# Optimization experiments

Hardware: AMD Instinct MI355X
Metric: run time of the kernel (lower is better)

The kernel has to match this reference:

```python
import jax, jax.numpy as jnp
import numpy as np

B, D, STRIDE, OUT = 8192, 1024, 16, 64
L = D // STRIDE


def setup_inputs() -> dict:
    key = jax.random.key(0)
    kx, kw, kb = jax.random.split(key, 3)
    x = jax.random.normal(kx, (B, D), dtype=jnp.float32)
    # Stacked per-layer Dense kernels: layer i only sees features j < i*STRIDE.
    # Glorot-ish scale; masked entries are zeroed in reference() (faithful: they
    # don't exist in the original per-layer kernels).
    W = jax.random.normal(kw, (L, D, OUT), dtype=jnp.float32) * 0.02
    b = jax.random.normal(kb, (L, OUT), dtype=jnp.float32) * 0.02
    return {"x": x, "W": W, "b": b}


def reference(x, W, b):
    # Original: tf.stack([Dense_i(x[..., :i*stride]) for i in range(L)], -2)
    # Equivalent single causal-masked batched matmul.
    Lx, Dx, Ox = W.shape
    stride = Dx // Lx
    # mask[l, d] = 1 if feature d is visible to layer l (d < l*stride)
    mask = (jnp.arange(Dx)[None, :] < (jnp.arange(Lx) * stride)[:, None]).astype(W.dtype)
    Wm = W * mask[:, :, None]                      # [L, D, O]
    out = jnp.einsum("bd,ldo->blo", x, Wm) + b    # [B, L, O]
    return out
```

## Files before the change

### kernel.cpp

```cpp
#include <hip/hip_runtime.h>
#include <hip/hip_bf16.h>
#include <stdint.h>

#define BROWS 8192
#define DDIM  1024
#define LDIM  64
#define ODIM  64
#define NDIM  4096
#define KSTRIDE 16

typedef __attribute__((ext_vector_type(8))) short bf16x8;
typedef __attribute__((ext_vector_type(4))) float f32x4;
typedef __attribute__((ext_vector_type(8))) unsigned short u16x8;

static __device__ __forceinline__ unsigned short f2bf(float f) {
    union { float f; uint32_t u; } v; v.f = f;
    uint32_t r = 0x7FFFu + ((v.u >> 16) & 1u);
    return (unsigned short)((v.u + r) >> 16);
}

static __device__ __forceinline__ void async16(const void* g, void* l) {
    __builtin_amdgcn_global_load_lds(
        (const __attribute__((address_space(1))) void*)g,
        (__attribute__((address_space(3))) void*)l, 16, 0, 0);
}

__global__ __launch_bounds__(256) void prep_kernel(const float* __restrict__ x,
                                                   const float* __restrict__ W,
                                                   unsigned short* __restrict__ xb,
                                                   unsigned short* __restrict__ wbt) {
    const int bid = blockIdx.x;
    if (bid < 1024) {
        __shared__ float tile[64][65];
        const int l  = bid >> 4;
        const int d0 = (bid & 15) << 6;
        const int t  = threadIdx.x;
        {
            const int dd = t >> 2;
            const int o4 = (t & 3) << 4;
            const float* src = W + ((size_t)((l << 10) + d0 + dd) << 6) + o4;
            #pragma unroll
            for (int j = 0; j < 4; ++j) {
                float4 v = reinterpret_cast<const float4*>(src)[j];
                tile[dd][o4 + 4 * j + 0] = v.x;
                tile[dd][o4 + 4 * j + 1] = v.y;
                tile[dd][o4 + 4 * j + 2] = v.z;
                tile[dd][o4 + 4 * j + 3] = v.w;
            }
        }
        __syncthreads();
        {
            const int o    = t >> 2;
            const int dloc = (t & 3) << 4;
            const int kmax = l * KSTRIDE;
            unsigned short* dst = wbt + ((size_t)((l << 6) + o) << 10) + d0 + dloc;
            u16x8 r0, r1;
            #pragma unroll
            for (int j = 0; j < 8; ++j) {
                int da = d0 + dloc + j;
                int db = da + 8;
                r0[j] = (da < kmax) ? f2bf(tile[dloc + j][o])     : (unsigned short)0;
                r1[j] = (db < kmax) ? f2bf(tile[dloc + 8 + j][o]) : (unsigned short)0;
            }
            *reinterpret_cast<u16x8*>(dst)     = r0;
            *reinterpret_cast<u16x8*>(dst + 8) = r1;
        }
    } else {
        int i = (bid - 1024) * 256 + threadIdx.x;
        const float4* xf = reinterpret_cast<const float4*>(x);
        float4 v0 = xf[2 * i];
        float4 v1 = xf[2 * i + 1];
        u16x8 r;
        r[0] = f2bf(v0.x); r[1] = f2bf(v0.y); r[2] = f2bf(v0.z); r[3] = f2bf(v0.w);
        r[4] = f2bf(v1.x); r[5] = f2bf(v1.y); r[6] = f2bf(v1.z); r[7] = f2bf(v1.w);
        reinterpret_cast<u16x8*>(xb)[i] = r;
    }
}

#define MMQ(A, B) \
    _Pragma("unroll") \
    for (int m = 0; m < 4; ++m) \
    _Pragma("unroll") \
    for (int n = 0; n < 4; ++n) \
        acc[m][n] = __builtin_amdgcn_mfma_f32_16x16x32_bf16(A[m], B[n], acc[m][n], 0, 0, 0);

#define READF(T, A, B) do { \
    const char* pb_ = lds + ((T) % 3) * 24576; \
    _Pragma("unroll") \
    for (int m = 0; m < 4; ++m) A[m] = *reinterpret_cast<const bf16x8*>(pb_ + aoff + m * 1024); \
    _Pragma("unroll") \
    for (int n = 0; n < 4; ++n) B[n] = *reinterpret_cast<const bf16x8*>(pb_ + boff + n * 1024); \
} while (0)

#define PHASE(T, Acur, Bcur, Anxt, Bnxt) \
    asm volatile("s_waitcnt vmcnt(3)" ::: "memory");    \
    __builtin_amdgcn_sched_barrier(0); \
    __builtin_amdgcn_s_barrier();                       \
    stage((T) + 3);                                     \
    READF((T) + 1, Anxt, Bnxt);                         \
    __builtin_amdgcn_sched_barrier(0); \
    __builtin_amdgcn_s_setprio(1); \
    MMQ(Acur, Bcur); \
    __builtin_amdgcn_s_setprio(0); \
    asm volatile("s_waitcnt lgkmcnt(0)" ::: "memory");

__global__ __launch_bounds__(512)
__attribute__((amdgpu_waves_per_eu(2)))
void ar_gemm_kernel(const unsigned short* __restrict__ xb,
                    const unsigned short* __restrict__ wbt,
                    const float* __restrict__ bias,
                    float* __restrict__ out) {
    __shared__ char lds[73728];

    const int s  = blockIdx.x >> 8;
    const int i  = blockIdx.x & 255;
    const int bm = ((s & 1) << 4) + (i & 15);
    const int bn = ((s < 2) ? 16 : 0) + 15 - (i >> 4);
    const int tid  = threadIdx.x;
    const int lane = tid & 63;
    const int wid  = tid >> 6;
    const int wm   = wid >> 1;
    const int wn   = wid & 1;

    const int nkt = bn + 1;

    const int cb = (tid & 3) << 4;
    const char* gA = (const char*)xb  + ((size_t)((bm << 8) + (tid >> 2)) << 11) + cb;
    const char* gB = (const char*)wbt + ((size_t)((bn << 7) + (tid >> 2)) << 11) + cb;

    const int aoff = ((wm << 6) + (lane & 15)) * 64 + ((lane >> 4) << 4);
    const int boff = 16384 + ((wn << 6) + (lane & 15)) * 64 + ((lane >> 4) << 4);

    f32x4 acc[4][4];
    #pragma unroll
    for (int m = 0; m < 4; ++m)
        #pragma unroll
        for (int n = 0; n < 4; ++n)
            acc[m][n] = (f32x4)(0.f);

    bf16x8 aA[4], bA[4], aB[4], bB[4];

    auto stage = [&](int t) {
        const int kb = (t < nkt ? t : nkt - 1) << 6;
        char* l = lds + (t % 3) * 24576 + tid * 16;
        async16(gA + kb, l);
        async16(gA + ((size_t)128 << 11) + kb, l + 8192);
        async16(gB + kb, l + 16384);
    };

    stage(0); stage(1); stage(2);
    asm volatile("s_waitcnt vmcnt(6)" ::: "memory");
    __builtin_amdgcn_s_barrier();
    READF(0, aA, bA);
    asm volatile("s_waitcnt lgkmcnt(0)" ::: "memory");

    int t = 0;
    while (true) {
        PHASE(t, aA, bA, aB, bB);
        if (++t >= nkt) break;
        PHASE(t, aB, bB, aA, bA);
        if (++t >= nkt) break;
    }
    asm volatile("s_waitcnt vmcnt(0)" ::: "memory");

    const int crow = (bm << 8) + (wm << 6) + ((lane >> 4) << 2);
    const int ccol = (bn << 7) + (wn << 6) + (lane & 15);
    float bv[4];
    #pragma unroll
    for (int n = 0; n < 4; ++n) bv[n] = bias[ccol + n * 16];
    #pragma unroll
    for (int m = 0; m < 4; ++m)
        #pragma unroll
        for (int n = 0; n < 4; ++n)
            #pragma unroll
            for (int j = 0; j < 4; ++j)
                out[(size_t)(crow + m * 16 + j) * NDIM + ccol + n * 16] = acc[m][n][j] + bv[n];
}

__global__ __launch_bounds__(256) void naive_kernel(const float* __restrict__ x,
                                                    const float* __restrict__ W,
                                                    const float* __restrict__ bias,
                                                    float* __restrict__ out) {
    size_t idx = (size_t)blockIdx.x * 256 + threadIdx.x;
    if (idx >= (size_t)BROWS * NDIM) return;
    int m = (int)(idx >> 12);
    int n = (int)(idx & 4095);
    int l = n >> 6;
    int o = n & 63;
    int kmax = l * KSTRIDE;
    float s = bias[n];
    const float* xr = x + (size_t)m * DDIM;
    const float* wp = W + ((size_t)l << 16) + o;
    for (int d = 0; d < kmax; ++d) s += xr[d] * wp[(size_t)d << 6];
    out[idx] = s;
}

extern "C" void kernel_launch(void* const* d_in, const int* in_sizes, int n_in,
                              void* d_out, int out_size, void* d_ws, size_t ws_size,
                              hipStream_t stream) {
    const float* x = (const float*)d_in[0];
    const float* W = (const float*)d_in[1];
    const float* b = (const float*)d_in[2];
    float* out = (float*)d_out;

    const size_t need = ((size_t)BROWS * DDIM + (size_t)NDIM * DDIM) * sizeof(unsigned short);
    if (ws_size < need) {
        int total = BROWS * NDIM;
        naive_kernel<<<(total + 255) / 256, 256, 0, stream>>>(x, W, b, out);
        return;
    }
    unsigned short* xbuf = (unsigned short*)d_ws;
    unsigned short* wbt  = xbuf + (size_t)BROWS * DDIM;

    prep_kernel<<<5120, 256, 0, stream>>>(x, W, xbuf, wbt);
    ar_gemm_kernel<<<1024, 512, 0, stream>>>(xbuf, wbt, b, out);
}
```

Before: 69.59 us.

## Shrink GEMM tile to 128x128, load B fragments straight from global into registers

The GEMM moves from 256x128 tiles with 512 threads to 128x128 tiles with 256 threads, and the grid doubles to 2048 blocks. Only the A (x) tile is staged through LDS with async loads into a 3-deep buffer. Each wave now reads its B (weight) fragments directly from global memory into double-buffered registers. This cuts LDS use and traffic and should allow more resident blocks per CU. In exchange, the weight tile is no longer shared between waves through LDS, so global loads of W rise, and the smaller tiles lower arithmetic intensity.

```diff
diff --git a/kernel.cpp b/kernel.cpp
--- a/kernel.cpp
+++ b/kernel.cpp
@@ -77,45 +77,38 @@
     }
 }
 
-#define MMQ(A, B) \
+#define ITER(T, BC, BN) do { \
+    stageA((T) + 2);                                    \
+    loadB((T) + 1, BN);                                 \
+    const char* pb_ = lds + ((T) % 3) * 8192; \
+    bf16x8 a[4]; \
+    _Pragma("unroll") \
+    for (int m = 0; m < 4; ++m) a[m] = *reinterpret_cast<const bf16x8*>(pb_ + aoff + m * 1024); \
+    __builtin_amdgcn_s_setprio(1); \
     _Pragma("unroll") \
     for (int m = 0; m < 4; ++m) \
-    _Pragma("unroll") \
-    for (int n = 0; n < 4; ++n) \
-        acc[m][n] = __builtin_amdgcn_mfma_f32_16x16x32_bf16(A[m], B[n], acc[m][n], 0, 0, 0);
-
-#define READF(T, A, B) do { \
-    const char* pb_ = lds + ((T) % 3) * 24576; \
-    _Pragma("unroll") \
-    for (int m = 0; m < 4; ++m) A[m] = *reinterpret_cast<const bf16x8*>(pb_ + aoff + m * 1024); \
-    _Pragma("unroll") \
-    for (int n = 0; n < 4; ++n) B[n] = *reinterpret_cast<const bf16x8*>(pb_ + boff + n * 1024); \
+        _Pragma("unroll") \
+        for (int n = 0; n < 4; ++n) \
+            acc[m][n] = __builtin_amdgcn_mfma_f32_16x16x32_bf16(a[m], BC[n], acc[m][n], 0, 0, 0); \
+    __builtin_amdgcn_s_setprio(0); \
+    asm volatile("s_waitcnt lgkmcnt(0)" ::: "memory");  \
+    asm volatile("s_waitcnt vmcnt(6)" ::: "memory");    \
+    __builtin_amdgcn_sched_barrier(0); \
+    __builtin_amdgcn_s_barrier(); \
+    __builtin_amdgcn_sched_barrier(0); \
 } while (0)
 
-#define PHASE(T, Acur, Bcur, Anxt, Bnxt) \
-    asm volatile("s_waitcnt vmcnt(3)" ::: "memory");    \
-    __builtin_amdgcn_sched_barrier(0); \
-    __builtin_amdgcn_s_barrier();                       \
-    stage((T) + 3);                                     \
-    READF((T) + 1, Anxt, Bnxt);                         \
-    __builtin_amdgcn_sched_barrier(0); \
-    __builtin_amdgcn_s_setprio(1); \
-    MMQ(Acur, Bcur); \
-    __builtin_amdgcn_s_setprio(0); \
-    asm volatile("s_waitcnt lgkmcnt(0)" ::: "memory");
-
-__global__ __launch_bounds__(512)
-__attribute__((amdgpu_waves_per_eu(2)))
-void ar_gemm_kernel(const unsigned short* __restrict__ xb,
-                    const unsigned short* __restrict__ wbt,
-                    const float* __restrict__ bias,
-                    float* __restrict__ out) {
-    __shared__ char lds[73728];
+__global__ __launch_bounds__(256, 3) void ar_gemm_kernel(
+        const unsigned short* __restrict__ xb,
+        const unsigned short* __restrict__ wbt,
+        const float* __restrict__ bias,
+        float* __restrict__ out) {
+    __shared__ char lds[24576];
 
     const int s  = blockIdx.x >> 8;
     const int i  = blockIdx.x & 255;
-    const int bm = ((s & 1) << 4) + (i & 15);
-    const int bn = ((s < 2) ? 16 : 0) + 15 - (i >> 4);
+    const int bm = ((s & 3) << 4) + (i & 15);
+    const int bn = ((s < 4) ? 16 : 0) + 15 - (i >> 4);
     const int tid  = threadIdx.x;
     const int lane = tid & 63;
     const int wid  = tid >> 6;
@@ -124,12 +117,14 @@
 
     const int nkt = bn + 1;
 
-    const int cb = (tid & 3) << 4;
-    const char* gA = (const char*)xb  + ((size_t)((bm << 8) + (tid >> 2)) << 11) + cb;
-    const char* gB = (const char*)wbt + ((size_t)((bn << 7) + (tid >> 2)) << 11) + cb;
-
+    const char* gA1 = (const char*)xb + ((size_t)((bm << 7) + (tid >> 2)) << 11) + ((tid & 3) << 4);
+    const char* gA2 = gA1 + ((size_t)64 << 11);
+    const char* gB[4];
+    #pragma unroll
+    for (int n = 0; n < 4; ++n)
+        gB[n] = (const char*)wbt + ((size_t)((bn << 7) + (wn << 6) + (n << 4) + (lane & 15)) << 11)
+              + ((lane >> 4) << 4);
     const int aoff = ((wm << 6) + (lane & 15)) * 64 + ((lane >> 4) << 4);
-    const int boff = 16384 + ((wn << 6) + (lane & 15)) * 64 + ((lane >> 4) << 4);
 
     f32x4 acc[4][4];
     #pragma unroll
@@ -138,32 +133,35 @@
         for (int n = 0; n < 4; ++n)
             acc[m][n] = (f32x4)(0.f);
 
-    bf16x8 aA[4], bA[4], aB[4], bB[4];
-
-    auto stage = [&](int t) {
+    auto stageA = [&](int t) {
         const int kb = (t < nkt ? t : nkt - 1) << 6;
-        char* l = lds + (t % 3) * 24576 + tid * 16;
-        async16(gA + kb, l);
-        async16(gA + ((size_t)128 << 11) + kb, l + 8192);
-        async16(gB + kb, l + 16384);
+        char* l = lds + (t % 3) * 8192 + tid * 16;
+        async16(gA1 + kb, l);
+        async16(gA2 + kb, l + 4096);
     };
-
-    stage(0); stage(1); stage(2);
+    auto loadB = [&](int t, bf16x8 (&b)[4]) {
+        const int kb = (t < nkt ? t : nkt - 1) << 6;
+        #pragma unroll
+        for (int n = 0; n < 4; ++n)
+            b[n] = *reinterpret_cast<const bf16x8*>(gB[n] + kb);
+    };
+
+    bf16x8 b0[4], b1[4];
+    stageA(0); stageA(1);
+    loadB(0, b0);
     asm volatile("s_waitcnt vmcnt(6)" ::: "memory");
     __builtin_amdgcn_s_barrier();
-    READF(0, aA, bA);
-    asm volatile("s_waitcnt lgkmcnt(0)" ::: "memory");
 
     int t = 0;
     while (true) {
-        PHASE(t, aA, bA, aB, bB);
+        ITER(t, b0, b1);
         if (++t >= nkt) break;
-        PHASE(t, aB, bB, aA, bA);
+        ITER(t, b1, b0);
         if (++t >= nkt) break;
     }
     asm volatile("s_waitcnt vmcnt(0)" ::: "memory");
 
-    const int crow = (bm << 8) + (wm << 6) + ((lane >> 4) << 2);
+    const int crow = (bm << 7) + (wm << 6) + ((lane >> 4) << 2);
     const int ccol = (bn << 7) + (wn << 6) + (lane & 15);
     float bv[4];
     #pragma unroll
@@ -213,5 +211,5 @@
     unsigned short* wbt  = xbuf + (size_t)BROWS * DDIM;
 
     prep_kernel<<<5120, 256, 0, stream>>>(x, W, xbuf, wbt);
-    ar_gemm_kernel<<<1024, 512, 0, stream>>>(xbuf, wbt, b, out);
-}
+    ar_gemm_kernel<<<2048, 256, 0, stream>>>(xbuf, wbt, b, out);
+}
```

Result: slower. 117.6 us (+69.0%).
